# Kernel optimization log

Hardware: AMD Instinct MI355X
Metric: run time of the kernel (lower is better)

## Reference

```python
import jax, jax.numpy as jnp
import numpy as np

EPS = 1e-6
LAMB = 0.1
ITERS = 3


def setup_inputs() -> dict:
    key = jax.random.key(0)
    k = jax.random.split(key, 6)
    bi, bt, R, W, D = 128, 128, 36, 50, 1024
    return {
        "img_cls": jax.random.normal(k[0], (bi, D), jnp.float32),
        "imgs": jax.random.normal(k[1], (bi, R, D), jnp.float32),
        "cap_cls": jax.random.normal(k[2], (bt, D), jnp.float32),
        "caps": jax.random.normal(k[3], (bt, W, D), jnp.float32),
        "img_lens": jax.random.randint(k[4], (bi,), 1, R + 1, jnp.int32),
        "cap_lens": jax.random.randint(k[5], (bt,), 1, W + 1, jnp.int32),
    }


def _bregman(cost, mask, r, c):
    # P = exp(-cost/lamb) (masked entries have cost=+inf -> P=0), then
    # iterative row/col rescaling toward marginals r, c.
    P = jnp.where(mask, jnp.exp(-cost / LAMB), 0.0)
    P = P / (jnp.sum(P, axis=(-2, -1), keepdims=True) + EPS)
    for _ in range(ITERS):
        u = P.sum(axis=-1) + EPS          # [bi,bt,R]
        P = P * (r / u)[..., None]
        v = P.sum(axis=-2) + EPS          # [bi,bt,W]
        P = P * (c / v)[:, :, None, :]
    return P


def reference(img_cls, imgs, cap_cls, caps, img_lens, cap_lens):
    imgs = imgs + EPS
    caps = caps + EPS
    # prepend cls token
    imgs = jnp.concatenate([img_cls[:, None, :], imgs], axis=1)   # [bi,R+1,D]
    caps = jnp.concatenate([cap_cls[:, None, :], caps], axis=1)   # [bt,W+1,D]
    imgs = imgs / jnp.linalg.norm(imgs, axis=-1, keepdims=True)
    caps = caps / jnp.linalg.norm(caps, axis=-1, keepdims=True)
    # fine-grained cosine sims: [bi, bt, R+1, W+1]
    fg_sims = jnp.einsum("ird,twd->itrw", imgs, caps)
    il = img_lens + 1
    cl = cap_lens + 1
    R1, W1 = imgs.shape[1], caps.shape[1]
    rmask = jnp.arange(R1)[None, :] < il[:, None]   # [bi,R+1]
    wmask = jnp.arange(W1)[None, :] < cl[:, None]   # [bt,W+1]
    mask = rmask[:, None, :, None] & wmask[None, :, None, :]  # [bi,bt,R+1,W+1]
    # _ave_init: uniform marginals over valid rows/cols
    rvalid = mask.any(axis=-1).astype(fg_sims.dtype)  # [bi,bt,R+1]
    cvalid = mask.any(axis=-2).astype(fg_sims.dtype)  # [bi,bt,W+1]
    r = rvalid / rvalid.sum(axis=-1, keepdims=True)
    c = cvalid / cvalid.sum(axis=-1, keepdims=True)
    cost = 1.0 - fg_sims
    tp = _bregman(cost, mask, r, c)
    sims = jnp.sum(fg_sims * tp * mask.astype(fg_sims.dtype), axis=(-2, -1))
    return sims  # [bi, bt]
```

## Files before the change

kernel.cpp:

```cpp
#include <hip/hip_runtime.h>
#include <hip/hip_fp16.h>

#define EPSF 1e-6f

typedef _Float16 f16x8 __attribute__((ext_vector_type(8)));
typedef float f32x4 __attribute__((ext_vector_type(4)));

#define BK 32
#define SMEM_BYTES 37888
#define BUF_BYTES 10240

#define AS1 __attribute__((address_space(1)))
#define AS3 __attribute__((address_space(3)))

#define VM_WAIT(N) asm volatile("s_waitcnt vmcnt(" #N ")" ::: "memory")
#define LGKM0()    asm volatile("s_waitcnt lgkmcnt(0)" ::: "memory")

template <int CTRL>
__device__ __forceinline__ float dpp_add(float x) {
    int y = __builtin_amdgcn_update_dpp(0, __float_as_int(x), CTRL, 0xf, 0xf, true);
    return x + __int_as_float(y);
}

__device__ __forceinline__ float wave_sum_bc(float x) {
    x = dpp_add<0xB1>(x);
    x = dpp_add<0x4E>(x);
    x = dpp_add<0x141>(x);
    x = dpp_add<0x140>(x);
    x = dpp_add<0x142>(x);
    x = dpp_add<0x143>(x);
    return __int_as_float(__builtin_amdgcn_readlane(__float_as_int(x), 63));
}

__global__ __launch_bounds__(256) void norm_kernel(
        const float* __restrict__ img_cls, const float* __restrict__ imgs,
        const float* __restrict__ cap_cls, const float* __restrict__ caps,
        __half* __restrict__ Ah, __half* __restrict__ Bh) {
    __shared__ float red[4];
    const int row = blockIdx.x;
    const int tid = threadIdx.x;

    const float* src = nullptr;
    __half* dsth;
    float eps_add = EPSF;
    if (row < 64 * 80) {
        const int g = row / 80, r = row % 80;
        dsth = Ah + (size_t)row * 1024 + tid * 4;
        int i = -1, rr = 0;
        if (r < 37)      { i = 2 * g;     rr = r; }
        else if (r < 74) { i = 2 * g + 1; rr = r - 37; }
        if (i >= 0) {
            if (rr == 0) { src = img_cls + (size_t)i * 1024; eps_add = 0.0f; }
            else         { src = imgs + ((size_t)i * 36 + (rr - 1)) * 1024; }
        }
    } else {
        const int row2 = row - 64 * 80;
        const int t = row2 >> 6, r = row2 & 63;
        const int n = r >> 4, fr = r & 15;
        const int kt = tid >> 3, q4 = (tid >> 1) & 3, j = (tid & 1) * 4;
        dsth = Bh + ((size_t)(t * 32 + kt) * 4 + n) * 512 + (q4 * 16 + fr) * 8 + j;
        if (r == 0)       { src = cap_cls + (size_t)t * 1024; eps_add = 0.0f; }
        else if (r <= 50) { src = caps + ((size_t)t * 50 + (r - 1)) * 1024; }
    }

    if (src == nullptr) {
        ushort4 z; z.x = z.y = z.z = z.w = 0;
        *reinterpret_cast<ushort4*>(dsth) = z;
        return;
    }

    float4 v = reinterpret_cast<const float4*>(src)[tid];
    v.x += eps_add; v.y += eps_add; v.z += eps_add; v.w += eps_add;
    float ss = v.x * v.x + v.y * v.y + v.z * v.z + v.w * v.w;
    #pragma unroll
    for (int m = 1; m <= 32; m <<= 1) ss += __shfl_xor(ss, m);
    if ((tid & 63) == 0) red[tid >> 6] = ss;
    __syncthreads();
    const float tot = red[0] + red[1] + red[2] + red[3];
    const float rn = 1.0f / sqrtf(tot);

    ushort4 o;
    o.x = __half_as_ushort(__float2half(v.x * rn));
    o.y = __half_as_ushort(__float2half(v.y * rn));
    o.z = __half_as_ushort(__float2half(v.z * rn));
    o.w = __half_as_ushort(__float2half(v.w * rn));
    *reinterpret_cast<ushort4*>(dsth) = o;
}

__device__ __forceinline__ void stage_octA(const __half* __restrict__ Ag,
                                           __half* buf, int kb, int o, size_t lofs) {
    const __half* src = Ag + (size_t)o * 16384 + kb + lofs;
    __builtin_amdgcn_global_load_lds((const AS1 void*)src,
                                     (AS3 void*)(buf + o * 512), 16, 0, 0);
}

__device__ __forceinline__ void stage_A(const __half* __restrict__ Ag,
                                        __half* buf, int kb, int wave, size_t lofs) {
    stage_octA(Ag, buf, kb, wave, lofs);
    stage_octA(Ag, buf, kb, wave + 4, lofs);
    if (wave < 2) stage_octA(Ag, buf, kb, wave + 8, lofs);
}

__device__ __forceinline__ void ds_af(const __half* buf, int wm, int fr, int q4,
                                      f16x8 af[5]) {
    const int soff = ((q4 ^ ((fr >> 1) & 3)) * 8);
    #pragma unroll
    for (int m = 0; m < 5; ++m) {
        const int R = wm * 80 + m * 16 + fr;
        af[m] = *reinterpret_cast<const f16x8*>(buf + R * BK + soff);
    }
}

__device__ __forceinline__ void load_bf(const __half* __restrict__ Bgw, int kt,
                                        f16x8 bf[4]) {
    const __half* p = Bgw + (size_t)kt * 2048;
    #pragma unroll
    for (int n = 0; n < 4; ++n)
        bf[n] = *reinterpret_cast<const f16x8*>(p + n * 512);
}

__device__ __forceinline__ void mfma_cluster(f32x4 acc[5][4], const f16x8 af[5],
                                             const f16x8 bf[4]) {
    __builtin_amdgcn_s_setprio(1);
    #pragma unroll
    for (int m = 0; m < 5; ++m)
        #pragma unroll
        for (int n = 0; n < 4; ++n)
            acc[m][n] = __builtin_amdgcn_mfma_f32_16x16x32_f16(af[m], bf[n], acc[m][n], 0, 0, 0);
    __builtin_amdgcn_s_setprio(0);
}

__global__ __launch_bounds__(256, 3) void fused_kernel(
        const __half* __restrict__ Ah, const __half* __restrict__ Bh,
        const int* __restrict__ img_lens, const int* __restrict__ cap_lens,
        float* __restrict__ out) {
    __shared__ __align__(16) char smem[SMEM_BYTES];
    __half* lds0 = reinterpret_cast<__half*>(smem);
    __half* lds1 = reinterpret_cast<__half*>(smem + BUF_BYTES);

    const int idx = blockIdx.x;
    const int xcd = idx & 7;
    const int within = idx >> 3;
    const int bx = within >> 3;
    const int by = xcd * 8 + (within & 7);

    const int tid = threadIdx.x;
    const int wave = tid >> 6;
    const int lane = tid & 63;
    const int wm = wave >> 1, wn = wave & 1;
    const int fr = lane & 15;
    const int q4 = lane >> 4;

    const __half* Ag = Ah + (size_t)bx * 160 * 1024;
    const __half* Bgw = Bh + (size_t)(2 * by + wn) * 65536 + lane * 8;

    const int rsub = lane >> 2;
    const int segsrc = (lane & 3) ^ ((lane >> 3) & 3);
    const size_t lofs = (size_t)rsub * 1024 + (size_t)(segsrc * 8);

    f32x4 acc[5][4];
    #pragma unroll
    for (int m = 0; m < 5; ++m)
        #pragma unroll
        for (int n = 0; n < 4; ++n) {
            f32x4 z = {0.0f, 0.0f, 0.0f, 0.0f};
            acc[m][n] = z;
        }

    f16x8 bfA[4], bfB[4];

    load_bf(Bgw, 0, bfA);
    stage_A(Ag, lds0, 0, wave, lofs);
    stage_A(Ag, lds1, BK, wave, lofs);
    load_bf(Bgw, 1, bfB);
    if (wave < 2) { VM_WAIT(7); } else { VM_WAIT(6); }
    __builtin_amdgcn_s_barrier();

    #define GEMM_TILE(KT, LDSBUF, CUR)                                \
    {                                                                 \
        f16x8 af[5];                                                  \
        ds_af((LDSBUF), wm, fr, q4, af);                              \
        mfma_cluster(acc, af, (CUR));                                 \
        load_bf(Bgw, (KT) + 2, (CUR));                                \
        LGKM0();                                                      \
        __builtin_amdgcn_s_barrier();                                 \
        stage_A(Ag, (LDSBUF), ((KT) + 2) * BK, wave, lofs);           \
        if (wave < 2) { VM_WAIT(7); } else { VM_WAIT(6); }            \
        __builtin_amdgcn_s_barrier();                                 \
    }

    #pragma unroll 1
    for (int kt = 0; kt < 30; kt += 2) {
        GEMM_TILE(kt, lds0, bfA);
        GEMM_TILE(kt + 1, lds1, bfB);
    }
    #undef GEMM_TILE

    {
        f16x8 af[5];
        ds_af(lds0, wm, fr, q4, af);
        mfma_cluster(acc, af, bfA);
        VM_WAIT(0);
        __builtin_amdgcn_s_barrier();
    }
    {
        f16x8 af[5];
        ds_af(lds1, wm, fr, q4, af);
        mfma_cluster(acc, af, bfB);
    }

    __syncthreads();

    float* fg = reinterpret_cast<float*>(smem) + wave * (37 * 64);
    const int orow = q4 * 4;

    #pragma unroll
    for (int p = 0; p < 2; ++p) {
        if (p) {
            LGKM0();
        }
        #pragma unroll
        for (int pm = 0; pm < 3; ++pm) {
            #pragma unroll
            for (int q = 0; q < 4; ++q) {
                const int lrow = (p ? 32 : 0) + pm * 16 + orow + q;
                const int srow = lrow - (p ? 37 : 0);
                const bool ok = p ? (lrow >= 37 && lrow < 74) : (lrow < 37);
                const int sw = ((srow >> 2) & 3) << 4;
                #pragma unroll
                for (int n = 0; n < 4; ++n)
                    if (ok) fg[srow * 64 + ((n * 16 + fr) ^ sw)] = acc[pm + 2 * p][n][q];
            }
        }

        const int i = 4 * bx + 2 * wm + p;
        const int t = 2 * by + wn;
        const int il = img_lens[i] + 1;
        const int cl = cap_lens[t] + 1;
        const bool vcol = lane < cl;

        #define FGR(r_) fg[(r_) * 64 + (lane ^ ((((r_) >> 2) & 3) << 4))]

        float P[37];
        float ts[4] = {0.f, 0.f, 0.f, 0.f};
        #pragma unroll
        for (int r = 0; r < 37; ++r) {
            if (r < il) {
                const float f = FGR(r);
                const float pe = vcol ? __expf((f - 1.0f) * 10.0f) : 0.0f;
                P[r] = pe;
                ts[r & 3] += pe;
            } else {
                P[r] = 0.0f;
            }
        }
        float tot = (ts[0] + ts[1]) + (ts[2] + ts[3]);
        tot = wave_sum_bc(tot);
        const float s0 = __builtin_amdgcn_rcpf(tot + EPSF);
        #pragma unroll
        for (int r = 0; r < 37; ++r) P[r] *= s0;

        const float rmarg = 1.0f / (float)il;
        const float cmarg = 1.0f / (float)cl;
        for (int it = 0; it < 3; ++it) {
            #pragma unroll
            for (int r = 0; r < 37; ++r) {
                if (r < il) {
                    const float u = wave_sum_bc(P[r]);
                    P[r] *= rmarg * __builtin_amdgcn_rcpf(u + EPSF);
                }
            }
            float vs[4] = {EPSF, 0.f, 0.f, 0.f};
            #pragma unroll
            for (int r = 0; r < 37; ++r) vs[r & 3] += P[r];
            const float v = (vs[0] + vs[1]) + (vs[2] + vs[3]);
            const float cs = vcol ? cmarg * __builtin_amdgcn_rcpf(v) : 0.0f;
            #pragma unroll
            for (int r = 0; r < 37; ++r) P[r] *= cs;
        }

        float ls[4] = {0.f, 0.f, 0.f, 0.f};
        #pragma unroll
        for (int r = 0; r < 37; ++r) {
            if (r < il) ls[r & 3] += FGR(r) * P[r];
        }
        float local = (ls[0] + ls[1]) + (ls[2] + ls[3]);
        local = wave_sum_bc(local);
        if (lane == 0) out[i * 128 + t] = local;
        #undef FGR
    }
}

extern "C" void kernel_launch(void* const* d_in, const int* in_sizes, int n_in,
                              void* d_out, int out_size, void* d_ws, size_t ws_size,
                              hipStream_t stream) {
    const float* img_cls  = (const float*)d_in[0];
    const float* imgs     = (const float*)d_in[1];
    const float* cap_cls  = (const float*)d_in[2];
    const float* caps     = (const float*)d_in[3];
    const int*   img_lens = (const int*)d_in[4];
    const int*   cap_lens = (const int*)d_in[5];
    float* out = (float*)d_out;

    __half* Ah = (__half*)d_ws;
    __half* Bh = Ah + (size_t)64 * 80 * 1024;

    norm_kernel<<<64 * 80 + 128 * 64, 256, 0, stream>>>(img_cls, imgs, cap_cls, caps, Ah, Bh);
    fused_kernel<<<2048, 256, 0, stream>>>(Ah, Bh, img_lens, cap_lens, out);
}
```

Baseline: 160.8 us.

## Quad-buffer A tiles in LDS to drop one barrier per k-step

Adds two more LDS buffers so A staging runs three tiles ahead. Each k-step now waits on a single barrier instead of two. The aim is to cut synchronisation stalls and hide global-load latency in the GEMM main loop. LDS use grows from 37888 to 40960 bytes, which may reduce occupancy at 3 blocks per CU. The epilogue vmcnt bookkeeping is also more intricate and could be mis-tuned.

Measured after the change: 159.9 us. No clear change (-0.6%).

```diff
diff --git a/kernel.cpp b/kernel.cpp
--- a/kernel.cpp
+++ b/kernel.cpp
@@ -7,7 +7,7 @@
 typedef float f32x4 __attribute__((ext_vector_type(4)));
 
 #define BK 32
-#define SMEM_BYTES 37888
+#define SMEM_BYTES 40960
 #define BUF_BYTES 10240
 
 #define AS1 __attribute__((address_space(1)))
@@ -137,6 +137,8 @@
     __shared__ __align__(16) char smem[SMEM_BYTES];
     __half* lds0 = reinterpret_cast<__half*>(smem);
     __half* lds1 = reinterpret_cast<__half*>(smem + BUF_BYTES);
+    __half* lds2 = reinterpret_cast<__half*>(smem + 2 * BUF_BYTES);
+    __half* lds3 = reinterpret_cast<__half*>(smem + 3 * BUF_BYTES);
 
     const int idx = blockIdx.x;
     const int xcd = idx & 7;
@@ -169,43 +171,57 @@
 
     f16x8 bfA[4], bfB[4];
 
+    stage_A(Ag, lds0, 0, wave, lofs);
     load_bf(Bgw, 0, bfA);
-    stage_A(Ag, lds0, 0, wave, lofs);
     stage_A(Ag, lds1, BK, wave, lofs);
     load_bf(Bgw, 1, bfB);
-    if (wave < 2) { VM_WAIT(7); } else { VM_WAIT(6); }
+    stage_A(Ag, lds2, 2 * BK, wave, lofs);
+    if (wave < 2) { VM_WAIT(10); } else { VM_WAIT(8); }
     __builtin_amdgcn_s_barrier();
 
-    #define GEMM_TILE(KT, LDSBUF, CUR)                                \
+    #define GEMM_TILE(KT, RDBUF, STBUF, CUR)                          \
     {                                                                 \
         f16x8 af[5];                                                  \
-        ds_af((LDSBUF), wm, fr, q4, af);                              \
+        ds_af((RDBUF), wm, fr, q4, af);                               \
         mfma_cluster(acc, af, (CUR));                                 \
         load_bf(Bgw, (KT) + 2, (CUR));                                \
         LGKM0();                                                      \
+        stage_A(Ag, (STBUF), ((KT) + 3) * BK, wave, lofs);            \
+        if (wave < 2) { VM_WAIT(10); } else { VM_WAIT(8); }           \
         __builtin_amdgcn_s_barrier();                                 \
-        stage_A(Ag, (LDSBUF), ((KT) + 2) * BK, wave, lofs);           \
-        if (wave < 2) { VM_WAIT(7); } else { VM_WAIT(6); }            \
-        __builtin_amdgcn_s_barrier();                                 \
     }
 
     #pragma unroll 1
-    for (int kt = 0; kt < 30; kt += 2) {
-        GEMM_TILE(kt, lds0, bfA);
-        GEMM_TILE(kt + 1, lds1, bfB);
-    }
+    for (int kt = 0; kt < 28; kt += 4) {
+        GEMM_TILE(kt,     lds0, lds3, bfA);
+        GEMM_TILE(kt + 1, lds1, lds0, bfB);
+        GEMM_TILE(kt + 2, lds2, lds1, bfA);
+        GEMM_TILE(kt + 3, lds3, lds2, bfB);
+    }
+    GEMM_TILE(28, lds0, lds3, bfA);
     #undef GEMM_TILE
 
-    {
-        f16x8 af[5];
-        ds_af(lds0, wm, fr, q4, af);
-        mfma_cluster(acc, af, bfA);
-        VM_WAIT(0);
-        __builtin_amdgcn_s_barrier();
-    }
     {
         f16x8 af[5];
         ds_af(lds1, wm, fr, q4, af);
+        mfma_cluster(acc, af, bfB);
+        load_bf(Bgw, 31, bfB);
+        LGKM0();
+        if (wave < 2) { VM_WAIT(7); } else { VM_WAIT(6); }
+        __builtin_amdgcn_s_barrier();
+    }
+    {
+        f16x8 af[5];
+        ds_af(lds2, wm, fr, q4, af);
+        mfma_cluster(acc, af, bfA);
+        LGKM0();
+        VM_WAIT(4);
+        __builtin_amdgcn_s_barrier();
+    }
+    {
+        f16x8 af[5];
+        ds_af(lds3, wm, fr, q4, af);
+        VM_WAIT(0);
         mfma_cluster(acc, af, bfB);
     }
 
```
